# Performance work log

Measured on AMD Instinct MI355X. Metric: run time of the kernel, lower is better.

The kernel has to match this reference:

```python
import jax, jax.numpy as jnp
import numpy as np

NUM_NODES = 50000
NUM_RELATIONS = 16
NUM_EDGES = 800000
HIDDEN = 64
NUM_CLASSES = 16


def setup_inputs() -> dict:
    key = jax.random.key(0)
    ks = jax.random.split(key, 8)
    edge_index = jax.random.randint(ks[0], (2, NUM_EDGES), 0, NUM_NODES, dtype=jnp.int32)
    edge_type = jax.random.randint(ks[1], (NUM_EDGES,), 0, NUM_RELATIONS, dtype=jnp.int32)
    node_emb = jax.random.normal(ks[2], (NUM_NODES, HIDDEN), dtype=jnp.float32) * 0.1
    W1 = jax.random.normal(ks[3], (NUM_RELATIONS, HIDDEN, HIDDEN), dtype=jnp.float32) * 0.1
    root1 = jax.random.normal(ks[4], (HIDDEN, HIDDEN), dtype=jnp.float32) * 0.1
    b1 = jnp.zeros((HIDDEN,), dtype=jnp.float32)
    W2 = jax.random.normal(ks[5], (NUM_RELATIONS, HIDDEN, NUM_CLASSES), dtype=jnp.float32) * 0.1
    root2 = jax.random.normal(ks[6], (HIDDEN, NUM_CLASSES), dtype=jnp.float32) * 0.1
    b2 = jnp.zeros((NUM_CLASSES,), dtype=jnp.float32)
    return {"edge_index": edge_index, "edge_type": edge_type, "node_emb": node_emb,
            "W1": W1, "root1": root1, "b1": b1, "W2": W2, "root2": root2, "b2": b2}


def rgcn_conv(x, src, dst, edge_type, W, root, bias, num_nodes):
    # PyG RGCNConv (aggr='mean', root_weight=True, bias=True, num_bases=None):
    # per relation r: transform all nodes, gather at src, scatter-MEAN at dst
    # (mean over edges of that relation per target node); sum over relations;
    # then add root transform and bias.
    out_dim = W.shape[-1]

    def body(acc, rw):
        W_r, r = rw
        h = x @ W_r                                   # [N, out]
        mask = (edge_type == r).astype(x.dtype)       # [E]
        msg = h[src] * mask[:, None]                  # [E, out]
        summed = jax.ops.segment_sum(msg, dst, num_segments=num_nodes)  # [N, out]
        cnt = jax.ops.segment_sum(mask, dst, num_segments=num_nodes)    # [N]
        mean = jnp.where(cnt[:, None] > 0, summed / jnp.maximum(cnt, 1.0)[:, None], 0.0)
        return acc + mean, None

    acc0 = jnp.zeros((num_nodes, out_dim), dtype=x.dtype)
    agg, _ = jax.lax.scan(body, acc0, (W, jnp.arange(W.shape[0])))
    return agg + x @ root + bias


def reference(edge_index, edge_type, node_emb, W1, root1, b1, W2, root2, b2):
    src, dst = edge_index[0], edge_index[1]
    n = node_emb.shape[0]
    x = rgcn_conv(node_emb, src, dst, edge_type, W1, root1, b1, n)
    x = jax.nn.relu(x)  # dropout p=0.0 -> identity
    x = rgcn_conv(x, src, dst, edge_type, W2, root2, b2, n)
    return x
```

## Files before the change

### kernel.cpp

```cpp
#include <hip/hip_runtime.h>
#include <hip/hip_bf16.h>

#define N_NODES 50000
#define NREL 16
#define HID 64
#define NCLS 16
#define NBKT (N_NODES * NREL)
#define SB 2048
#define NSB ((NBKT + SB - 1) / SB)
#define TILE 32
#define NTB ((N_NODES + TILE - 1) / TILE)
#define PGRID 256
#define XCHUNKS (N_NODES * HID / 8)
#define W1N (17 * HID * HID)
#define W2N (17 * NCLS * HID)

typedef __attribute__((ext_vector_type(8))) short bf16x8;
typedef __attribute__((ext_vector_type(4))) float f32x4;
typedef __attribute__((ext_vector_type(2))) int i32x2;

static __device__ __forceinline__ unsigned short f2bf(float f) {
    __hip_bfloat16 h = __float2bfloat16(f);
    return *reinterpret_cast<unsigned short*>(&h);
}
static __device__ __forceinline__ float bf2f(unsigned short u) {
    __hip_bfloat16 h;
    *reinterpret_cast<unsigned short*>(&h) = u;
    return __bfloat162float(h);
}

#define MFMA16(A, B, C) __builtin_amdgcn_mfma_f32_16x16x32_bf16((A), (B), (C), 0, 0, 0)

#define LD128A(D, P) \
    asm volatile("global_load_dwordx4 %0, %1, off" : "=v"(D) : "v"((const void*)(P)) : "memory")
#define LD64A(D, P) \
    asm volatile("global_load_dwordx2 %0, %1, off" : "=v"(D) : "v"((const void*)(P)) : "memory")
#define VWAIT0()                                           \
    do {                                                   \
        asm volatile("s_waitcnt vmcnt(0)" ::: "memory");   \
        __builtin_amdgcn_sched_barrier(0);                 \
    } while (0)


__global__ __launch_bounds__(256) void pre_k(const int* __restrict__ dstp,
                                             const int* __restrict__ et,
                                             int* __restrict__ bcnt,
                                             int* __restrict__ rank, int E,
                                             const float* __restrict__ x,
                                             const float* __restrict__ W1,
                                             const float* __restrict__ root1,
                                             const float* __restrict__ W2,
                                             const float* __restrict__ root2,
                                             ushort* __restrict__ xb,
                                             ushort* __restrict__ WbT1,
                                             ushort* __restrict__ WbT2) {
    int eb = (E + 255) >> 8;
    if ((int)blockIdx.x < eb) {
        int i = blockIdx.x * 256 + threadIdx.x;
        if (i < E) {
            int b = dstp[i] * NREL + et[i];
            rank[i] = atomicAdd(&bcnt[b], 1);
        }
        return;
    }
    int i = (blockIdx.x - eb) * 256 + threadIdx.x;
    if (i < XCHUNKS) {
        float4 f0 = *(const float4*)(x + (size_t)i * 8);
        float4 f1 = *(const float4*)(x + (size_t)i * 8 + 4);
        bf16x8 o;
        o[0] = (short)f2bf(f0.x); o[1] = (short)f2bf(f0.y);
        o[2] = (short)f2bf(f0.z); o[3] = (short)f2bf(f0.w);
        o[4] = (short)f2bf(f1.x); o[5] = (short)f2bf(f1.y);
        o[6] = (short)f2bf(f1.z); o[7] = (short)f2bf(f1.w);
        *(bf16x8*)(xb + (size_t)i * 8) = o;
    } else {
        int j = i - XCHUNKS;
        if (j < W1N) {
            int t = j >> 12, rem = j & 4095, n = rem >> 6, k = rem & 63;
            float v = (t < 16) ? W1[(size_t)t * HID * HID + k * HID + n]
                               : root1[k * HID + n];
            WbT1[j] = f2bf(v);
        } else {
            int m = j - W1N;
            if (m < W2N) {
                int t = m >> 10, rem = m & 1023, n = rem >> 6, k = rem & 63;
                float v = (t < 16) ? W2[(size_t)t * HID * NCLS + k * NCLS + n]
                                   : root2[k * NCLS + n];
                WbT2[m] = f2bf(v);
            }
        }
    }
}

__global__ __launch_bounds__(256) void scan1_k(const int* __restrict__ bcnt,
                                               int* __restrict__ bsum) {
    int b = blockIdx.x, t = threadIdx.x;
    int base = b * SB + t * 8;
    int s = 0;
#pragma unroll
    for (int j = 0; j < 8; ++j)
        if (base + j < NBKT) s += bcnt[base + j];
#pragma unroll
    for (int off = 1; off < 64; off <<= 1) s += __shfl_xor(s, off, 64);
    __shared__ int ws[4];
    if ((t & 63) == 0) ws[t >> 6] = s;
    __syncthreads();
    if (t == 0) bsum[b] = ws[0] + ws[1] + ws[2] + ws[3];
}

__global__ __launch_bounds__(512) void scan2_k(int* __restrict__ bsum,
                                               int* __restrict__ rstart, int E) {
    __shared__ int ts[512];
    int t = threadIdx.x;
    int v = (t < NSB) ? bsum[t] : 0;
    ts[t] = v;
    __syncthreads();
    int acc = v;
    for (int off = 1; off < 512; off <<= 1) {
        int u = (t >= off) ? ts[t - off] : 0;
        __syncthreads();
        acc += u;
        ts[t] = acc;
        __syncthreads();
    }
    if (t < NSB) bsum[t] = acc - v;
    if (t == 0) rstart[NBKT] = E;
}

__global__ __launch_bounds__(256) void scan3_k(int* __restrict__ bcnt,
                                               const int* __restrict__ bsum) {
    int b = blockIdx.x, t = threadIdx.x;
    int base = b * SB + t * 8;
    int a[8];
    int s = 0;
#pragma unroll
    for (int j = 0; j < 8; ++j) {
        a[j] = (base + j < NBKT) ? bcnt[base + j] : 0;
        s += a[j];
    }
    __shared__ int ts[256];
    ts[t] = s;
    __syncthreads();
    int acc = s;
    for (int off = 1; off < 256; off <<= 1) {
        int u = (t >= off) ? ts[t - off] : 0;
        __syncthreads();
        acc += u;
        ts[t] = acc;
        __syncthreads();
    }
    int run = bsum[b] + (acc - s);
#pragma unroll
    for (int j = 0; j < 8; ++j) {
        if (base + j < NBKT) bcnt[base + j] = run;
        run += a[j];
    }
}

__global__ __launch_bounds__(256) void scat_k(const int* __restrict__ srcp,
                                              const int* __restrict__ dstp,
                                              const int* __restrict__ et,
                                              const int* __restrict__ rank,
                                              const int* __restrict__ rstart,
                                              int2* __restrict__ sedge, int E) {
    int i = blockIdx.x * 256 + threadIdx.x;
    if (i < E) {
        int r = et[i];
        int b = dstp[i] * NREL + r;
        int lo = rstart[b], hi = rstart[b + 1];
        float inv = 1.0f / (float)(hi - lo);
        sedge[lo + rank[i]] = make_int2(srcp[i] | (r << 16), __float_as_int(inv));
    }
}


#define RSTART_LOAD(T, LO, HI)                                                \
    do {                                                                      \
        int node_ = (T) * TILE + g;                                           \
        LO = 0; HI = 0;                                                       \
        if (node_ < N_NODES) {                                                \
            int b0_ = node_ * NREL + h * 8;                                   \
            LO = rstart[b0_];                                                 \
            HI = rstart[b0_ + 8];                                             \
        }                                                                     \
    } while (0)

#define DESC_ISSUE(LO, HI)                                                    \
    do {                                                                      \
        int dg_ = (HI) - (LO);                                                \
        int bs_ = dg_ > 0 ? (LO) : 0;                                         \
        int lt_ = dg_ > 0 ? (HI)-1 : 0;                                       \
        _Pragma("unroll") for (int j_ = 0; j_ < 16; ++j_) {                   \
            int ix_ = bs_ + j_;                                               \
            if (ix_ > lt_) ix_ = lt_;                                         \
            LD64A(d[j_], sedge + ix_);                                        \
        }                                                                     \
    } while (0)

#define FEAT_ISSUE()                                                          \
    do {                                                                      \
        _Pragma("unroll") for (int j_ = 0; j_ < 16; ++j_)                     \
            LD128A(v[j_], xcol + (size_t)(d[j_].x & 0xFFFF) * HID);           \
    } while (0)

#define GFLUSHX(ABP)                                                          \
    {                                                                         \
        bf16x8 o_;                                                            \
        o_[0] = (short)f2bf(acc_[0]); o_[1] = (short)f2bf(acc_[1]);           \
        o_[2] = (short)f2bf(acc_[2]); o_[3] = (short)f2bf(acc_[3]);           \
        o_[4] = (short)f2bf(acc_[4]); o_[5] = (short)f2bf(acc_[5]);           \
        o_[6] = (short)f2bf(acc_[6]); o_[7] = (short)f2bf(acc_[7]);           \
        *(bf16x8*)((ABP) + ((curRel_ * (TILE * 128) + rowoff) ^ swg)) = o_;   \
        acc_[0] = 0.f; acc_[1] = 0.f; acc_[2] = 0.f; acc_[3] = 0.f;           \
        acc_[4] = 0.f; acc_[5] = 0.f; acc_[6] = 0.f; acc_[7] = 0.f;           \
    }

#define CONSUME(ABP, LO, HI)                                                  \
    do {                                                                      \
        char* abp_ = (char*)(ABP);                                            \
        int deg_ = (HI) - (LO);                                               \
        const bf16x8 zz_ = {0, 0, 0, 0, 0, 0, 0, 0};                          \
        _Pragma("unroll") for (int r_ = 0; r_ < 8; ++r_)                      \
            *(bf16x8*)(abp_ + (((h * 8 + r_) * (TILE * 128) + rowoff) ^ swg)) = zz_; \
        float acc_[8] = {0.f, 0.f, 0.f, 0.f, 0.f, 0.f, 0.f, 0.f};             \
        int curRel_ = h * 8;                                                  \
        _Pragma("unroll") for (int j_ = 0; j_ < 16; ++j_) {                   \
            if (j_ < deg_) {                                                  \
                int rr_ = (d[j_].x >> 16) & 15;                               \
                if (rr_ != curRel_) { GFLUSHX(abp_); curRel_ = rr_; }         \
                float iv_ = __int_as_float(d[j_].y);                          \
                _Pragma("unroll") for (int q_ = 0; q_ < 8; ++q_)              \
                    acc_[q_] = fmaf(iv_, bf2f((unsigned short)v[j_][q_]), acc_[q_]); \
            }                                                                 \
        }                                                                     \
        for (int e_ = (LO) + 16; e_ < (HI); ++e_) {            \
            int2 m_ = sedge[e_];                                              \
            int rr_ = (m_.x >> 16) & 15;                                      \
            if (rr_ != curRel_) { GFLUSHX(abp_); curRel_ = rr_; }             \
            float iv_ = __int_as_float(m_.y);                                 \
            bf16x8 vv_ = *(const bf16x8*)(xcol + (size_t)(m_.x & 0xFFFF) * HID); \
            _Pragma("unroll") for (int q_ = 0; q_ < 8; ++q_)                  \
                acc_[q_] = fmaf(iv_, bf2f((unsigned short)vv_[q_]), acc_[q_]); \
        }                                                                     \
        if (deg_ > 0) GFLUSHX(abp_);                                          \
    } while (0)

__global__ __launch_bounds__(512, 2) void fuse1_k(const ushort* __restrict__ xb,
                                                  const int2* __restrict__ sedge,
                                                  const int* __restrict__ rstart,
                                                  const ushort* __restrict__ WbT1,
                                                  const float* __restrict__ b1,
                                                  ushort* __restrict__ X1b) {
    __shared__ bf16x8 Abuf[2][NREL * TILE * 8];
    __shared__ float P[4][TILE][16];
    int tid = threadIdx.x, bid = blockIdx.x;
    int wave = tid >> 6, lane = tid & 63;
    int mr = lane & 15, kq = lane >> 4;
    int cg = wave & 3, th = wave >> 2;
    int grp = tid >> 3, l8 = tid & 7;
    int g = grp & 31, h = grp >> 5;
    int swg = (g & 7) << 4;
    int rowoff = (g << 7) + (l8 << 4);
    const ushort* xcol = xb + l8 * 8;
    int sw = (mr & 7) << 4;
    int a00o = ((mr << 7) + (kq << 4)) ^ sw;
    int a01o = ((mr << 7) + 64 + (kq << 4)) ^ sw;
    int a10o = (((16 + mr) << 7) + (kq << 4)) ^ sw;
    int a11o = (((16 + mr) << 7) + 64 + (kq << 4)) ^ sw;

    const ushort* wbase = WbT1 + (cg * 16 + mr) * HID + kq * 8;
    bf16x8 w0[8], w1[8];
#pragma unroll
    for (int i = 0; i < 8; ++i) {
        w0[i] = *(const bf16x8*)(wbase + (th * 8 + i) * 4096);
        w1[i] = *(const bf16x8*)(wbase + (th * 8 + i) * 4096 + 32);
    }
    bf16x8 wr0 = *(const bf16x8*)(wbase + 16 * 4096);
    bf16x8 wr1 = *(const bf16x8*)(wbase + 16 * 4096 + 32);
    float4 bv = *(const float4*)(b1 + ((tid * 4) & 63));

    i32x2 d[16];
    bf16x8 v[16];

    int lo, hi;
    RSTART_LOAD(bid, lo, hi);
    DESC_ISSUE(lo, hi);
    VWAIT0();
    FEAT_ISSUE();
    VWAIT0();
    CONSUME(&Abuf[0][0], lo, hi);
    int cur = 0;

    for (int k = 0;; ++k) {
        int tile = bid + k * PGRID;
        int dst0 = tile * TILE;
        bool hasNext = (tile + PGRID) < NTB;
        int nlo = 0, nhi = 0;
        if (hasNext) RSTART_LOAD(tile + PGRID, nlo, nhi);
        __syncthreads();
        if (hasNext) DESC_ISSUE(nlo, nhi);
        int r0 = dst0 + mr;      if (r0 >= N_NODES) r0 = N_NODES - 1;
        int r1 = dst0 + 16 + mr; if (r1 >= N_NODES) r1 = N_NODES - 1;
        bf16x8 ra00, ra01, ra10, ra11;
        LD128A(ra00, xb + (size_t)r0 * HID + kq * 8);
        LD128A(ra01, xb + (size_t)r0 * HID + kq * 8 + 32);
        LD128A(ra10, xb + (size_t)r1 * HID + kq * 8);
        LD128A(ra11, xb + (size_t)r1 * HID + kq * 8 + 32);

        const char* Abase = (const char*)&Abuf[cur][0] + th * (8 * TILE * 128);
        f32x4 c0 = {0.f, 0.f, 0.f, 0.f}, c1 = {0.f, 0.f, 0.f, 0.f};
#pragma unroll
        for (int i = 0; i < 4; ++i) {
            const char* At = Abase + i * (TILE * 128);
            bf16x8 a00 = *(const bf16x8*)(At + a00o);
            bf16x8 a01 = *(const bf16x8*)(At + a01o);
            bf16x8 a10 = *(const bf16x8*)(At + a10o);
            bf16x8 a11 = *(const bf16x8*)(At + a11o);
            c0 = MFMA16(a00, w0[i], c0);
            c0 = MFMA16(a01, w1[i], c0);
            c1 = MFMA16(a10, w0[i], c1);
            c1 = MFMA16(a11, w1[i], c1);
        }
        VWAIT0();
        if (hasNext) FEAT_ISSUE();
#pragma unroll
        for (int i = 4; i < 8; ++i) {
            const char* At = Abase + i * (TILE * 128);
            bf16x8 a00 = *(const bf16x8*)(At + a00o);
            bf16x8 a01 = *(const bf16x8*)(At + a01o);
            bf16x8 a10 = *(const bf16x8*)(At + a10o);
            bf16x8 a11 = *(const bf16x8*)(At + a11o);
            c0 = MFMA16(a00, w0[i], c0);
            c0 = MFMA16(a01, w1[i], c0);
            c1 = MFMA16(a10, w0[i], c1);
            c1 = MFMA16(a11, w1[i], c1);
        }
        if (th) {
            c0 = MFMA16(ra00, wr0, c0);
            c0 = MFMA16(ra01, wr1, c0);
            c1 = MFMA16(ra10, wr0, c1);
            c1 = MFMA16(ra11, wr1, c1);
        }
        if (th == 0) {
#pragma unroll
            for (int j = 0; j < 4; ++j) {
                P[cg][kq * 4 + j][mr] = c0[j];
                P[cg][16 + kq * 4 + j][mr] = c1[j];
            }
        }
        __syncthreads();
        if (th == 1) {
#pragma unroll
            for (int j = 0; j < 4; ++j) {
                P[cg][kq * 4 + j][mr] += c0[j];
                P[cg][16 + kq * 4 + j][mr] += c1[j];
            }
        }
        __syncthreads();
        {
            int idx = tid * 4, row = idx >> 6, colb = idx & 63;
            int node = dst0 + row;
            if (node < N_NODES) {
                f32x4 pv = *(const f32x4*)&P[colb >> 4][row][colb & 15];
                ushort4 o;
                o.x = f2bf(fmaxf(pv[0] + bv.x, 0.f));
                o.y = f2bf(fmaxf(pv[1] + bv.y, 0.f));
                o.z = f2bf(fmaxf(pv[2] + bv.z, 0.f));
                o.w = f2bf(fmaxf(pv[3] + bv.w, 0.f));
                *(ushort4*)(X1b + (size_t)node * HID + colb) = o;
            }
        }
        if (!hasNext) break;
        VWAIT0();
        CONSUME(&Abuf[cur ^ 1][0], nlo, nhi);
        cur ^= 1;
    }
}

__global__ __launch_bounds__(512, 2) void fuse2_k(const ushort* __restrict__ X1b,
                                                  const int2* __restrict__ sedge,
                                                  const int* __restrict__ rstart,
                                                  const ushort* __restrict__ WbT2,
                                                  const float* __restrict__ b2,
                                                  float* __restrict__ out) {
    __shared__ bf16x8 Abuf[2][NREL * TILE * 8];
    __shared__ float P[8][TILE][16];
    int tid = threadIdx.x, bid = blockIdx.x;
    int wave = tid >> 6, lane = tid & 63;
    int mr = lane & 15, kq = lane >> 4;
    int grp = tid >> 3, l8 = tid & 7;
    int g = grp & 31, h = grp >> 5;
    int swg = (g & 7) << 4;
    int rowoff = (g << 7) + (l8 << 4);
    const ushort* xcol = X1b + l8 * 8;
    int sw = (mr & 7) << 4;
    int a00o = ((mr << 7) + (kq << 4)) ^ sw;
    int a01o = ((mr << 7) + 64 + (kq << 4)) ^ sw;
    int a10o = (((16 + mr) << 7) + (kq << 4)) ^ sw;
    int a11o = (((16 + mr) << 7) + 64 + (kq << 4)) ^ sw;

    const ushort* wbase = WbT2 + mr * HID + kq * 8;
    bf16x8 uA0 = *(const bf16x8*)(wbase + wave * 1024);
    bf16x8 uA1 = *(const bf16x8*)(wbase + wave * 1024 + 32);
    bf16x8 uB0 = *(const bf16x8*)(wbase + (wave + 8) * 1024);
    bf16x8 uB1 = *(const bf16x8*)(wbase + (wave + 8) * 1024 + 32);
    bf16x8 wr0 = *(const bf16x8*)(wbase + 16 * 1024);
    bf16x8 wr1 = *(const bf16x8*)(wbase + 16 * 1024 + 32);
    float bc = b2[tid & 15];

    i32x2 d[16];
    bf16x8 v[16];

    int lo, hi;
    RSTART_LOAD(bid, lo, hi);
    DESC_ISSUE(lo, hi);
    VWAIT0();
    FEAT_ISSUE();
    VWAIT0();
    CONSUME(&Abuf[0][0], lo, hi);
    int cur = 0;

    for (int k = 0;; ++k) {
        int tile = bid + k * PGRID;
        int dst0 = tile * TILE;
        bool hasNext = (tile + PGRID) < NTB;
        int nlo = 0, nhi = 0;
        if (hasNext) RSTART_LOAD(tile + PGRID, nlo, nhi);
        __syncthreads();
        if (hasNext) DESC_ISSUE(nlo, nhi);
        int r0 = dst0 + mr;      if (r0 >= N_NODES) r0 = N_NODES - 1;
        int r1 = dst0 + 16 + mr; if (r1 >= N_NODES) r1 = N_NODES - 1;
        bf16x8 ra00, ra01, ra10, ra11;
        LD128A(ra00, X1b + (size_t)r0 * HID + kq * 8);
        LD128A(ra01, X1b + (size_t)r0 * HID + kq * 8 + 32);
        LD128A(ra10, X1b + (size_t)r1 * HID + kq * 8);
        LD128A(ra11, X1b + (size_t)r1 * HID + kq * 8 + 32);

        const char* Ab = (const char*)&Abuf[cur][0];
        f32x4 c0 = {0.f, 0.f, 0.f, 0.f}, c1 = {0.f, 0.f, 0.f, 0.f};
        {
            const char* At = Ab + wave * (TILE * 128);
            bf16x8 a00 = *(const bf16x8*)(At + a00o);
            bf16x8 a01 = *(const bf16x8*)(At + a01o);
            bf16x8 a10 = *(const bf16x8*)(At + a10o);
            bf16x8 a11 = *(const bf16x8*)(At + a11o);
            c0 = MFMA16(a00, uA0, c0);
            c0 = MFMA16(a01, uA1, c0);
            c1 = MFMA16(a10, uA0, c1);
            c1 = MFMA16(a11, uA1, c1);
        }
        VWAIT0();
        if (hasNext) FEAT_ISSUE();
        {
            const char* At = Ab + (wave + 8) * (TILE * 128);
            bf16x8 a00 = *(const bf16x8*)(At + a00o);
            bf16x8 a01 = *(const bf16x8*)(At + a01o);
            bf16x8 a10 = *(const bf16x8*)(At + a10o);
            bf16x8 a11 = *(const bf16x8*)(At + a11o);
            c0 = MFMA16(a00, uB0, c0);
            c0 = MFMA16(a01, uB1, c0);
            c1 = MFMA16(a10, uB0, c1);
            c1 = MFMA16(a11, uB1, c1);
        }
        if (wave == 7) {
            c0 = MFMA16(ra00, wr0, c0);
            c0 = MFMA16(ra01, wr1, c0);
            c1 = MFMA16(ra10, wr0, c1);
            c1 = MFMA16(ra11, wr1, c1);
        }
#pragma unroll
        for (int j = 0; j < 4; ++j) {
            P[wave][kq * 4 + j][mr] = c0[j];
            P[wave][16 + kq * 4 + j][mr] = c1[j];
        }
        __syncthreads();
        {
            int row = tid >> 4, cc = tid & 15;
            int node = dst0 + row;
            if (node < N_NODES) {
                float s = P[0][row][cc] + P[1][row][cc] + P[2][row][cc] +
                          P[3][row][cc] + P[4][row][cc] + P[5][row][cc] +
                          P[6][row][cc] + P[7][row][cc] + bc;
                out[(size_t)node * NCLS + cc] = s;
            }
        }
        if (!hasNext) break;
        VWAIT0();
        CONSUME(&Abuf[cur ^ 1][0], nlo, nhi);
        cur ^= 1;
    }
}

extern "C" void kernel_launch(void* const* d_in, const int* in_sizes, int n_in,
                              void* d_out, int out_size, void* d_ws, size_t ws_size,
                              hipStream_t stream) {
    const int* ei    = (const int*)d_in[0];
    const int* et    = (const int*)d_in[1];
    const float* x   = (const float*)d_in[2];
    const float* W1  = (const float*)d_in[3];
    const float* r1  = (const float*)d_in[4];
    const float* b1  = (const float*)d_in[5];
    const float* W2  = (const float*)d_in[6];
    const float* r2  = (const float*)d_in[7];
    const float* b2  = (const float*)d_in[8];
    float* out = (float*)d_out;

    int E = in_sizes[0] / 2;
    const int* srcp = ei;
    const int* dstp = ei + E;

    int*    bcnt  = (int*)d_ws;
    int*    rank  = bcnt + (NBKT + 20);
    int*    bsum  = rank + E;
    int2*   sedge = (int2*)(bsum + 512);
    ushort* WbT1  = (ushort*)(sedge + E);
    ushort* WbT2  = WbT1 + W1N;
    ushort* xb    = WbT2 + W2N;
    ushort* X1b   = xb + (size_t)N_NODES * HID;
    int*    rstart = bcnt;

    hipMemsetAsync(bcnt, 0, (NBKT + 20) * sizeof(int), stream);

    int eb = (E + 255) / 256;
    int cvtThreads = XCHUNKS + W1N + W2N;
    int cvtBlocks = (cvtThreads + 255) / 256;

    pre_k<<<eb + cvtBlocks, 256, 0, stream>>>(dstp, et, bcnt, rank, E,
                                              x, W1, r1, W2, r2, xb, WbT1, WbT2);
    scan1_k<<<NSB, 256, 0, stream>>>(bcnt, bsum);
    scan2_k<<<1, 512, 0, stream>>>(bsum, rstart, E);
    scan3_k<<<NSB, 256, 0, stream>>>(bcnt, bsum);
    scat_k<<<eb, 256, 0, stream>>>(srcp, dstp, et, rank, rstart, sedge, E);

    fuse1_k<<<PGRID, 512, 0, stream>>>(xb, sedge, rstart, WbT1, b1, X1b);
    fuse2_k<<<PGRID, 512, 0, stream>>>(X1b, sedge, rstart, WbT2, b2, out);
}
```

Baseline: 248.8 us.

## Merge scan kernels, use atomic cursors for scatter, restructure fuse2 as one-tile-per-block

```diff
diff --git a/kernel.cpp b/kernel.cpp
--- a/kernel.cpp
+++ b/kernel.cpp
@@ -44,8 +44,7 @@
 
 __global__ __launch_bounds__(256) void pre_k(const int* __restrict__ dstp,
                                              const int* __restrict__ et,
-                                             int* __restrict__ bcnt,
-                                             int* __restrict__ rank, int E,
+                                             int* __restrict__ bcnt, int E,
                                              const float* __restrict__ x,
                                              const float* __restrict__ W1,
                                              const float* __restrict__ root1,
@@ -57,10 +56,7 @@
     int eb = (E + 255) >> 8;
     if ((int)blockIdx.x < eb) {
         int i = blockIdx.x * 256 + threadIdx.x;
-        if (i < E) {
-            int b = dstp[i] * NREL + et[i];
-            rank[i] = atomicAdd(&bcnt[b], 1);
-        }
+        if (i < E) atomicAdd(&bcnt[dstp[i] * NREL + et[i]], 1);
         return;
     }
     int i = (blockIdx.x - eb) * 256 + threadIdx.x;
@@ -108,28 +104,20 @@
     if (t == 0) bsum[b] = ws[0] + ws[1] + ws[2] + ws[3];
 }
 
-__global__ __launch_bounds__(512) void scan2_k(int* __restrict__ bsum,
-                                               int* __restrict__ rstart, int E) {
-    __shared__ int ts[512];
-    int t = threadIdx.x;
-    int v = (t < NSB) ? bsum[t] : 0;
-    ts[t] = v;
+__global__ __launch_bounds__(256) void scan23_k(int* __restrict__ bcnt,
+                                                const int* __restrict__ bsum,
+                                                int* __restrict__ cursor, int E) {
+    int b = blockIdx.x, t = threadIdx.x;
+    int ps = 0;
+    for (int j = t; j < b; j += 256) ps += bsum[j];
+#pragma unroll
+    for (int off = 1; off < 64; off <<= 1) ps += __shfl_xor(ps, off, 64);
+    __shared__ int wps[4];
+    __shared__ int prefix;
+    if ((t & 63) == 0) wps[t >> 6] = ps;
     __syncthreads();
-    int acc = v;
-    for (int off = 1; off < 512; off <<= 1) {
-        int u = (t >= off) ? ts[t - off] : 0;
-        __syncthreads();
-        acc += u;
-        ts[t] = acc;
-        __syncthreads();
-    }
-    if (t < NSB) bsum[t] = acc - v;
-    if (t == 0) rstart[NBKT] = E;
-}
-
-__global__ __launch_bounds__(256) void scan3_k(int* __restrict__ bcnt,
-                                               const int* __restrict__ bsum) {
-    int b = blockIdx.x, t = threadIdx.x;
+    if (t == 0) prefix = wps[0] + wps[1] + wps[2] + wps[3];
+
     int base = b * SB + t * 8;
     int a[8];
     int s = 0;
@@ -149,27 +137,31 @@
         ts[t] = acc;
         __syncthreads();
     }
-    int run = bsum[b] + (acc - s);
+    int run = prefix + (acc - s);
 #pragma unroll
     for (int j = 0; j < 8; ++j) {
-        if (base + j < NBKT) bcnt[base + j] = run;
+        if (base + j < NBKT) {
+            bcnt[base + j] = run;
+            cursor[base + j] = run;
+        }
         run += a[j];
     }
+    if (b == 0 && t == 0) bcnt[NBKT] = E;
 }
 
 __global__ __launch_bounds__(256) void scat_k(const int* __restrict__ srcp,
                                               const int* __restrict__ dstp,
                                               const int* __restrict__ et,
-                                              const int* __restrict__ rank,
                                               const int* __restrict__ rstart,
+                                              int* __restrict__ cursor,
                                               int2* __restrict__ sedge, int E) {
     int i = blockIdx.x * 256 + threadIdx.x;
     if (i < E) {
         int r = et[i];
         int b = dstp[i] * NREL + r;
-        int lo = rstart[b], hi = rstart[b + 1];
-        float inv = 1.0f / (float)(hi - lo);
-        sedge[lo + rank[i]] = make_int2(srcp[i] | (r << 16), __float_as_int(inv));
+        int p = atomicAdd(&cursor[b], 1);
+        float inv = 1.0f / (float)(rstart[b + 1] - rstart[b]);
+        sedge[p] = make_int2(srcp[i] | (r << 16), __float_as_int(inv));
     }
 }
 
@@ -377,117 +369,159 @@
     }
 }
 
-__global__ __launch_bounds__(512, 2) void fuse2_k(const ushort* __restrict__ X1b,
+
+#define GFLUSH()                                                              \
+    {                                                                         \
+        bf16x8 o_;                                                            \
+        o_[0] = (short)f2bf(acc[0]); o_[1] = (short)f2bf(acc[1]);             \
+        o_[2] = (short)f2bf(acc[2]); o_[3] = (short)f2bf(acc[3]);             \
+        o_[4] = (short)f2bf(acc[4]); o_[5] = (short)f2bf(acc[5]);             \
+        o_[6] = (short)f2bf(acc[6]); o_[7] = (short)f2bf(acc[7]);             \
+        *(bf16x8*)(Ab + ((curRel * (TILE * 128) + rowoff) ^ sw)) = o_;        \
+        acc[0] = 0.f; acc[1] = 0.f; acc[2] = 0.f; acc[3] = 0.f;               \
+        acc[4] = 0.f; acc[5] = 0.f; acc[6] = 0.f; acc[7] = 0.f;               \
+    }
+
+static __device__ __forceinline__ void gather_tile(char* Ab,
+                                                   const ushort* __restrict__ ft,
+                                                   const int2* __restrict__ sedge,
+                                                   const int* __restrict__ rstart,
+                                                   int dst0, int tid) {
+    int g = tid >> 3, l8 = tid & 7;
+    int node = dst0 + g;
+    bool valid = node < N_NODES;
+
+    int lo = 0, hi = 0;
+    if (valid) {
+        lo = rstart[node * NREL];
+        hi = rstart[node * NREL + NREL];
+    }
+    int deg = hi - lo;
+    int base = (deg > 0) ? lo : 0;
+    int last = (deg > 0) ? hi - 1 : 0;
+
+    int sw = (g & 7) << 4;
+    int rowoff = (g << 7) + (l8 << 4);
+    const bf16x8 zz = {0, 0, 0, 0, 0, 0, 0, 0};
+
+    int2 d[32];
+#pragma unroll
+    for (int j = 0; j < 32; ++j) {
+        int idx = base + j;
+        if (idx > last) idx = last;
+        d[j] = sedge[idx];
+    }
+
+#pragma unroll
+    for (int t = 0; t < 16; ++t)
+        *(bf16x8*)(Ab + ((t * (TILE * 128) + rowoff) ^ sw)) = zz;
+    {
+        bf16x8 v = zz;
+        if (valid) v = *(const bf16x8*)(ft + (size_t)node * HID + l8 * 8);
+        *(bf16x8*)(Ab + ((16 * (TILE * 128) + rowoff) ^ sw)) = v;
+    }
+
+    const ushort* xcol = ft + l8 * 8;
+    bf16x8 v[32];
+#pragma unroll
+    for (int j = 0; j < 32; ++j)
+        v[j] = *(const bf16x8*)(xcol + (size_t)(d[j].x & 0xFFFF) * HID);
+    __builtin_amdgcn_sched_barrier(0);
+
+    float acc[8] = {0.f, 0.f, 0.f, 0.f, 0.f, 0.f, 0.f, 0.f};
+    int curRel = 0;
+#pragma unroll
+    for (int j = 0; j < 32; ++j) {
+        if (j < deg) {
+            int r_ = (d[j].x >> 16) & 15;
+            if (r_ != curRel) {
+                GFLUSH();
+                curRel = r_;
+            }
+            float inv_ = __int_as_float(d[j].y);
+#pragma unroll
+            for (int q = 0; q < 8; ++q)
+                acc[q] = fmaf(inv_, bf2f((unsigned short)v[j][q]), acc[q]);
+        }
+    }
+    for (int e = lo + 32; e < hi; ++e) {
+        int2 m = sedge[e];
+        int r = (m.x >> 16) & 15;
+        if (r != curRel) {
+            GFLUSH();
+            curRel = r;
+        }
+        float inv = __int_as_float(m.y);
+        bf16x8 vv = *(const bf16x8*)(xcol + (size_t)(m.x & 0xFFFF) * HID);
+#pragma unroll
+        for (int q = 0; q < 8; ++q)
+            acc[q] = fmaf(inv, bf2f((unsigned short)vv[q]), acc[q]);
+    }
+    if (deg > 0) GFLUSH();
+}
+
+__global__ __launch_bounds__(256, 2) void fuse2_k(const ushort* __restrict__ X1b,
                                                   const int2* __restrict__ sedge,
                                                   const int* __restrict__ rstart,
                                                   const ushort* __restrict__ WbT2,
                                                   const float* __restrict__ b2,
                                                   float* __restrict__ out) {
-    __shared__ bf16x8 Abuf[2][NREL * TILE * 8];
-    __shared__ float P[8][TILE][16];
-    int tid = threadIdx.x, bid = blockIdx.x;
+    __shared__ bf16x8 Abuf[17 * TILE * 8];
+    __shared__ float P[4 * TILE * NCLS];
+    char* Ab = (char*)Abuf;
+    int tid = threadIdx.x;
+    int dst0 = blockIdx.x * TILE;
+
+    gather_tile(Ab, X1b, sedge, rstart, dst0, tid);
+
     int wave = tid >> 6, lane = tid & 63;
     int mr = lane & 15, kq = lane >> 4;
-    int grp = tid >> 3, l8 = tid & 7;
-    int g = grp & 31, h = grp >> 5;
-    int swg = (g & 7) << 4;
-    int rowoff = (g << 7) + (l8 << 4);
-    const ushort* xcol = X1b + l8 * 8;
+    f32x4 c0 = {0.f, 0.f, 0.f, 0.f}, c1 = {0.f, 0.f, 0.f, 0.f};
+    const ushort* wb = WbT2 + mr * HID + kq * 8;
     int sw = (mr & 7) << 4;
     int a00o = ((mr << 7) + (kq << 4)) ^ sw;
     int a01o = ((mr << 7) + 64 + (kq << 4)) ^ sw;
     int a10o = (((16 + mr) << 7) + (kq << 4)) ^ sw;
     int a11o = (((16 + mr) << 7) + 64 + (kq << 4)) ^ sw;
 
-    const ushort* wbase = WbT2 + mr * HID + kq * 8;
-    bf16x8 uA0 = *(const bf16x8*)(wbase + wave * 1024);
-    bf16x8 uA1 = *(const bf16x8*)(wbase + wave * 1024 + 32);
-    bf16x8 uB0 = *(const bf16x8*)(wbase + (wave + 8) * 1024);
-    bf16x8 uB1 = *(const bf16x8*)(wbase + (wave + 8) * 1024 + 32);
-    bf16x8 wr0 = *(const bf16x8*)(wbase + 16 * 1024);
-    bf16x8 wr1 = *(const bf16x8*)(wbase + 16 * 1024 + 32);
-    float bc = b2[tid & 15];
-
-    i32x2 d[16];
-    bf16x8 v[16];
-
-    int lo, hi;
-    RSTART_LOAD(bid, lo, hi);
-    DESC_ISSUE(lo, hi);
-    VWAIT0();
-    FEAT_ISSUE();
-    VWAIT0();
-    CONSUME(&Abuf[0][0], lo, hi);
-    int cur = 0;
-
-    for (int k = 0;; ++k) {
-        int tile = bid + k * PGRID;
-        int dst0 = tile * TILE;
-        bool hasNext = (tile + PGRID) < NTB;
-        int nlo = 0, nhi = 0;
-        if (hasNext) RSTART_LOAD(tile + PGRID, nlo, nhi);
-        __syncthreads();
-        if (hasNext) DESC_ISSUE(nlo, nhi);
-        int r0 = dst0 + mr;      if (r0 >= N_NODES) r0 = N_NODES - 1;
-        int r1 = dst0 + 16 + mr; if (r1 >= N_NODES) r1 = N_NODES - 1;
-        bf16x8 ra00, ra01, ra10, ra11;
-        LD128A(ra00, X1b + (size_t)r0 * HID + kq * 8);
-        LD128A(ra01, X1b + (size_t)r0 * HID + kq * 8 + 32);
-        LD128A(ra10, X1b + (size_t)r1 * HID + kq * 8);
-        LD128A(ra11, X1b + (size_t)r1 * HID + kq * 8 + 32);
-
-        const char* Ab = (const char*)&Abuf[cur][0];
-        f32x4 c0 = {0.f, 0.f, 0.f, 0.f}, c1 = {0.f, 0.f, 0.f, 0.f};
-        {
-            const char* At = Ab + wave * (TILE * 128);
-            bf16x8 a00 = *(const bf16x8*)(At + a00o);
-            bf16x8 a01 = *(const bf16x8*)(At + a01o);
-            bf16x8 a10 = *(const bf16x8*)(At + a10o);
-            bf16x8 a11 = *(const bf16x8*)(At + a11o);
-            c0 = MFMA16(a00, uA0, c0);
-            c0 = MFMA16(a01, uA1, c0);
-            c1 = MFMA16(a10, uA0, c1);
-            c1 = MFMA16(a11, uA1, c1);
-        }
-        VWAIT0();
-        if (hasNext) FEAT_ISSUE();
-        {
-            const char* At = Ab + (wave + 8) * (TILE * 128);
-            bf16x8 a00 = *(const bf16x8*)(At + a00o);
-            bf16x8 a01 = *(const bf16x8*)(At + a01o);
-            bf16x8 a10 = *(const bf16x8*)(At + a10o);
-            bf16x8 a11 = *(const bf16x8*)(At + a11o);
-            c0 = MFMA16(a00, uB0, c0);
-            c0 = MFMA16(a01, uB1, c0);
-            c1 = MFMA16(a10, uB0, c1);
-            c1 = MFMA16(a11, uB1, c1);
-        }
-        if (wave == 7) {
-            c0 = MFMA16(ra00, wr0, c0);
-            c0 = MFMA16(ra01, wr1, c0);
-            c1 = MFMA16(ra10, wr0, c1);
-            c1 = MFMA16(ra11, wr1, c1);
-        }
-#pragma unroll
-        for (int j = 0; j < 4; ++j) {
-            P[wave][kq * 4 + j][mr] = c0[j];
-            P[wave][16 + kq * 4 + j][mr] = c1[j];
-        }
-        __syncthreads();
-        {
-            int row = tid >> 4, cc = tid & 15;
-            int node = dst0 + row;
-            if (node < N_NODES) {
-                float s = P[0][row][cc] + P[1][row][cc] + P[2][row][cc] +
-                          P[3][row][cc] + P[4][row][cc] + P[5][row][cc] +
-                          P[6][row][cc] + P[7][row][cc] + bc;
-                out[(size_t)node * NCLS + cc] = s;
-            }
-        }
-        if (!hasNext) break;
-        VWAIT0();
-        CONSUME(&Abuf[cur ^ 1][0], nlo, nhi);
-        cur ^= 1;
+    bf16x8 bk0 = *(const bf16x8*)(wb + wave * 1024);
+    bf16x8 bk1 = *(const bf16x8*)(wb + wave * 1024 + 32);
+    __syncthreads();
+
+    for (int t = wave; t < 17; t += 4) {
+        bf16x8 nb0 = bk0, nb1 = bk1;
+        if (t + 4 < 17) {
+            nb0 = *(const bf16x8*)(wb + (t + 4) * 1024);
+            nb1 = *(const bf16x8*)(wb + (t + 4) * 1024 + 32);
+        }
+        const char* At = Ab + t * (TILE * 128);
+        bf16x8 a00 = *(const bf16x8*)(At + a00o);
+        bf16x8 a01 = *(const bf16x8*)(At + a01o);
+        bf16x8 a10 = *(const bf16x8*)(At + a10o);
+        bf16x8 a11 = *(const bf16x8*)(At + a11o);
+        c0 = MFMA16(a00, bk0, c0);
+        c0 = MFMA16(a01, bk1, c0);
+        c1 = MFMA16(a10, bk0, c1);
+        c1 = MFMA16(a11, bk1, c1);
+        bk0 = nb0;
+        bk1 = nb1;
+    }
+    float* Pw = P + wave * (TILE * NCLS);
+#pragma unroll
+    for (int j = 0; j < 4; ++j) {
+        Pw[(kq * 4 + j) * NCLS + mr] = c0[j];
+        Pw[(16 + kq * 4 + j) * NCLS + mr] = c1[j];
+    }
+    __syncthreads();
+
+    int idx = tid * 2;
+    int row = idx >> 4, c = idx & 15;
+    float s0 = P[idx] + P[512 + idx] + P[1024 + idx] + P[1536 + idx] + b2[c];
+    float s1 = P[idx + 1] + P[512 + idx + 1] + P[1024 + idx + 1] +
+               P[1536 + idx + 1] + b2[c + 1];
+    if (dst0 + row < N_NODES) {
+        float2 o = make_float2(s0, s1);
+        *(float2*)(out + (size_t)(dst0 + row) * NCLS + c) = o;
     }
 }
 
@@ -509,14 +543,14 @@
     const int* srcp = ei;
     const int* dstp = ei + E;
 
-    int*    bcnt  = (int*)d_ws;
-    int*    rank  = bcnt + (NBKT + 20);
-    int*    bsum  = rank + E;
-    int2*   sedge = (int2*)(bsum + 512);
-    ushort* WbT1  = (ushort*)(sedge + E);
-    ushort* WbT2  = WbT1 + W1N;
-    ushort* xb    = WbT2 + W2N;
-    ushort* X1b   = xb + (size_t)N_NODES * HID;
+    int*    bcnt   = (int*)d_ws;
+    int*    cursor = bcnt + (NBKT + 20);
+    int*    bsum   = cursor + NBKT;
+    int2*   sedge  = (int2*)(bsum + 512);
+    ushort* WbT1   = (ushort*)(sedge + E);
+    ushort* WbT2   = WbT1 + W1N;
+    ushort* xb     = WbT2 + W2N;
+    ushort* X1b    = xb + (size_t)N_NODES * HID;
     int*    rstart = bcnt;
 
     hipMemsetAsync(bcnt, 0, (NBKT + 20) * sizeof(int), stream);
@@ -525,13 +559,12 @@
     int cvtThreads = XCHUNKS + W1N + W2N;
     int cvtBlocks = (cvtThreads + 255) / 256;
 
-    pre_k<<<eb + cvtBlocks, 256, 0, stream>>>(dstp, et, bcnt, rank, E,
+    pre_k<<<eb + cvtBlocks, 256, 0, stream>>>(dstp, et, bcnt, E,
                                               x, W1, r1, W2, r2, xb, WbT1, WbT2);
     scan1_k<<<NSB, 256, 0, stream>>>(bcnt, bsum);
-    scan2_k<<<1, 512, 0, stream>>>(bsum, rstart, E);
-    scan3_k<<<NSB, 256, 0, stream>>>(bcnt, bsum);
-    scat_k<<<eb, 256, 0, stream>>>(srcp, dstp, et, rank, rstart, sedge, E);
+    scan23_k<<<NSB, 256, 0, stream>>>(bcnt, bsum, cursor, E);
+    scat_k<<<eb, 256, 0, stream>>>(srcp, dstp, et, rstart, cursor, sedge, E);
 
     fuse1_k<<<PGRID, 512, 0, stream>>>(xb, sedge, rstart, WbT1, b1, X1b);
-    fuse2_k<<<PGRID, 512, 0, stream>>>(X1b, sedge, rstart, WbT2, b2, out);
-}
+    fuse2_k<<<NTB, 256, 0, stream>>>(X1b, sedge, rstart, WbT2, b2, out);
+}
```

Result: slower. 259.8 us (+4.4%).
